# Kernel tuning notes

Hardware: AMD Instinct MI355X
Metric: run time of the kernel (lower is better)

The kernel has to match this reference:

```python
import jax, jax.numpy as jnp
import numpy as np

B, S, T, D = 4, 512, 512, 256


def setup_inputs() -> dict:
    key = jax.random.key(0)
    ks = jax.random.split(key, 10)
    scale = 1.0 / np.sqrt(D)
    return {
        "source": jax.random.normal(ks[0], (B, S, D), jnp.float32),
        "target": jax.random.normal(ks[1], (B, T, D), jnp.float32),
        "W_src": jax.random.uniform(ks[2], (D, D), jnp.float32, -scale, scale),
        "b_src": jax.random.uniform(ks[3], (D,), jnp.float32, -scale, scale),
        "W_tgt": jax.random.uniform(ks[4], (D, D), jnp.float32, -scale, scale),
        "b_tgt": jax.random.uniform(ks[5], (D,), jnp.float32, -scale, scale),
        "W_res": jax.random.uniform(ks[6], (D, 1), jnp.float32, -scale, scale),
        "b_res": jax.random.uniform(ks[7], (1,), jnp.float32, -scale, scale),
        "W_prob": jax.random.uniform(ks[8], (D, 2), jnp.float32, -scale, scale),
        "b_prob": jax.random.uniform(ks[9], (2,), jnp.float32, -scale, scale),
    }


def reference(source, target, W_src, b_src, W_tgt, b_tgt, W_res, b_res, W_prob, b_prob):
    # source: (B,S,D), target: (B,T,D)
    src_lin = jnp.einsum("bsd,de->bse", source, W_src) + b_src  # (B,S,D)
    tgt_lin = jnp.einsum("btd,de->bte", target, W_tgt) + b_tgt  # (B,T,D)
    # Bahdanau-style additive attention: (B,T,S,D) broadcast, tanh, D->1
    h = jnp.tanh(src_lin[:, None, :, :] + tgt_lin[:, :, None, :])  # (B,T,S,D)
    genP = jnp.einsum("btsd,d->bts", h, W_res[:, 0]) + b_res[0]     # (B,T,S)
    prob = jax.nn.softmax(jnp.einsum("btd,de->bte", target, W_prob) + b_prob, axis=-1)  # (B,T,2)
    return genP, prob
```

## Files before the change

### kernel.cpp

```cpp
#include <hip/hip_runtime.h>

#define B_ 4
#define S_ 512
#define T_ 512
#define D_ 256
#define NSRC (B_ * S_)
#define K2F 2.8853900817779268f

typedef __attribute__((ext_vector_type(8))) short short8;
typedef __attribute__((ext_vector_type(4))) float f32x4;

__device__ __forceinline__ unsigned short f2bf(float f) {
    union { float f; unsigned u; } v; v.f = f;
    unsigned r = v.u + 0x7FFF + ((v.u >> 16) & 1);
    return (unsigned short)(r >> 16);
}

__global__ __launch_bounds__(256) void prep_kernel(
    const float* __restrict__ src, const float* __restrict__ tgt,
    const float* __restrict__ Wsrc, const float* __restrict__ Wtgt,
    const float* __restrict__ Wp, const float* __restrict__ bp,
    unsigned short* __restrict__ abf, unsigned short* __restrict__ wtb,
    float* __restrict__ out)
{
    __shared__ float tl[64 * 65];
    const int blk = blockIdx.x, tid = threadIdx.x;

    if (blk < 1024) {
        int i4 = blk * 256 + tid;
        const int half = NSRC * D_ / 4;
        const float4* in = (i4 < half) ? (const float4*)src : (const float4*)tgt;
        int j = (i4 < half) ? i4 : i4 - half;
        float4 v = in[j];
        ushort4 o;
        o.x = f2bf(v.x); o.y = f2bf(v.y); o.z = f2bf(v.z); o.w = f2bf(v.w);
        *(ushort4*)&abf[i4 * 4] = o;
    } else if (blk < 1056) {
        int wb = blk - 1024;
        int e = wb >> 4, ti = wb & 15, tr = ti >> 2, tc = ti & 3;
        int r0 = tr * 64, c0 = tc * 64;
        const float* W = e ? Wtgt : Wsrc;
        #pragma unroll
        for (int it = 0; it < 4; it++) {
            int rr = (tid >> 4) + it * 16;
            int cc = (tid & 15) * 4;
            float4 v = *(const float4*)&W[(r0 + rr) * D_ + c0 + cc];
            tl[(cc + 0) * 65 + rr] = v.x;
            tl[(cc + 1) * 65 + rr] = v.y;
            tl[(cc + 2) * 65 + rr] = v.z;
            tl[(cc + 3) * 65 + rr] = v.w;
        }
        __syncthreads();
        #pragma unroll
        for (int it = 0; it < 2; it++) {
            int jj = (tid >> 3) + it * 32;
            int kk = (tid & 7) * 8;
            ushort4 lo, hi;
            lo.x = f2bf(tl[jj * 65 + kk + 0]); lo.y = f2bf(tl[jj * 65 + kk + 1]);
            lo.z = f2bf(tl[jj * 65 + kk + 2]); lo.w = f2bf(tl[jj * 65 + kk + 3]);
            hi.x = f2bf(tl[jj * 65 + kk + 4]); hi.y = f2bf(tl[jj * 65 + kk + 5]);
            hi.z = f2bf(tl[jj * 65 + kk + 6]); hi.w = f2bf(tl[jj * 65 + kk + 7]);
            int idx = (e * 256 + c0 + jj) * D_ + r0 + kk;
            *(ushort4*)&wtb[idx] = lo;
            *(ushort4*)&wtb[idx + 4] = hi;
        }
    } else {
        int row  = (blk - 1056) * 4 + (tid >> 6);
        int lane = tid & 63;
        float p0 = 0.f, p1 = 0.f;
        #pragma unroll
        for (int i = 0; i < 4; i++) {
            int d = lane + i * 64;
            float v = tgt[row * D_ + d];
            float2 w = *(const float2*)&Wp[d * 2];
            p0 = fmaf(v, w.x, p0);
            p1 = fmaf(v, w.y, p1);
        }
        #pragma unroll
        for (int off = 32; off > 0; off >>= 1) {
            p0 += __shfl_down(p0, off, 64);
            p1 += __shfl_down(p1, off, 64);
        }
        if (lane == 0) {
            const float L2E = 1.4426950408889634f;
            float l0 = p0 + bp[0], l1 = p1 + bp[1];
            float e10 = __builtin_amdgcn_exp2f((l1 - l0) * L2E);
            float e01 = __builtin_amdgcn_exp2f((l0 - l1) * L2E);
            out[B_ * T_ * S_ + row * 2 + 0] = __builtin_amdgcn_rcpf(1.f + e10);
            out[B_ * T_ * S_ + row * 2 + 1] = __builtin_amdgcn_rcpf(1.f + e01);
        }
    }
}

__global__ __launch_bounds__(256, 1) void mega_kernel(
    const unsigned short* __restrict__ abf, const unsigned short* __restrict__ wtb,
    const float* __restrict__ bsrc, const float* __restrict__ btgt,
    const float* __restrict__ Wres, const float* __restrict__ bres,
    float* __restrict__ out)
{
    __shared__ float ls[64 * 68];
    __shared__ float lt[64 * 68];
    __shared__ float wl[D_];
    __shared__ float c0s;

    const int tid = threadIdx.x;
    const int lane = tid & 63, w = tid >> 6;
    const int s0 = blockIdx.x * 64;
    const int t0 = blockIdx.y * 64;
    const int b  = blockIdx.z;

    wl[tid] = Wres[tid];
    if (w == 0) {
        float s = Wres[lane] + Wres[lane + 64] + Wres[lane + 128] + Wres[lane + 192];
        #pragma unroll
        for (int off = 32; off > 0; off >>= 1) s += __shfl_xor(s, off, 64);
        if (lane == 0) c0s = s + bres[0];
    }

    const int mat  = w >> 1;
    const int half = w & 1;
    const int n = lane & 15, quad = lane >> 4;
    const float* bias = mat ? btgt : bsrc;
    float* lx = mat ? lt : ls;
    const int R = mat ? (NSRC + b * T_ + t0) : (b * S_ + s0);

    short8 af[4][8];
    #pragma unroll
    for (int rg = 0; rg < 4; rg++)
        #pragma unroll
        for (int ks = 0; ks < 8; ks++)
            af[rg][ks] = *(const short8*)&abf[(R + rg * 16 + n) * D_ + ks * 32 + quad * 8];

    const int m = tid & 15;
    const int g = tid >> 4;
    float acc[4][4];
    #pragma unroll
    for (int i = 0; i < 4; i++)
        #pragma unroll
        for (int j = 0; j < 4; j++) acc[i][j] = 0.f;

    for (int c = 0; c < 4; c++) {
        #pragma unroll
        for (int cgi = 0; cgi < 2; cgi++) {
            const int cg = half * 2 + cgi;
            const int gcol = c * 4 + cg;
            const unsigned short* bptr = &wtb[(mat * 256 + gcol * 16 + n) * D_ + quad * 8];
            short8 bf[8];
            #pragma unroll
            for (int ks = 0; ks < 8; ks++) bf[ks] = *(const short8*)&bptr[ks * 32];
            const int dloc = cg * 16 + n;
            const float bv = bias[gcol * 16 + n];
            #pragma unroll
            for (int rg = 0; rg < 4; rg++) {
                f32x4 a4 = {0.f, 0.f, 0.f, 0.f};
                #pragma unroll
                for (int ks = 0; ks < 8; ks++)
                    a4 = __builtin_amdgcn_mfma_f32_16x16x32_bf16(af[rg][ks], bf[ks], a4, 0, 0, 0);
                float4 o;
                o.x = __builtin_amdgcn_exp2f((a4[0] + bv) * K2F);
                o.y = __builtin_amdgcn_exp2f((a4[1] + bv) * K2F);
                o.z = __builtin_amdgcn_exp2f((a4[2] + bv) * K2F);
                o.w = __builtin_amdgcn_exp2f((a4[3] + bv) * K2F);
                *(float4*)&lx[dloc * 68 + rg * 16 + quad * 4] = o;
            }
        }
        __syncthreads();

        const float* wp = &wl[c * 64];
        #pragma unroll 8
        for (int k = 0; k < 64; k++) {
            float4 av = *(const float4*)&ls[k * 68 + 4 * m];
            float4 cv = *(const float4*)&lt[k * 68 + 4 * g];
            float wv = wp[k];
            float a0 = av.x, a1 = av.y, a2 = av.z, a3 = av.w;
            float c0 = cv.x, c1 = cv.y, c2 = cv.z, c3 = cv.w;
            float r;
            r = __builtin_amdgcn_rcpf(fmaf(c0, a0, 1.f)); acc[0][0] = fmaf(wv, r, acc[0][0]);
            r = __builtin_amdgcn_rcpf(fmaf(c0, a1, 1.f)); acc[0][1] = fmaf(wv, r, acc[0][1]);
            r = __builtin_amdgcn_rcpf(fmaf(c0, a2, 1.f)); acc[0][2] = fmaf(wv, r, acc[0][2]);
            r = __builtin_amdgcn_rcpf(fmaf(c0, a3, 1.f)); acc[0][3] = fmaf(wv, r, acc[0][3]);
            r = __builtin_amdgcn_rcpf(fmaf(c1, a0, 1.f)); acc[1][0] = fmaf(wv, r, acc[1][0]);
            r = __builtin_amdgcn_rcpf(fmaf(c1, a1, 1.f)); acc[1][1] = fmaf(wv, r, acc[1][1]);
            r = __builtin_amdgcn_rcpf(fmaf(c1, a2, 1.f)); acc[1][2] = fmaf(wv, r, acc[1][2]);
            r = __builtin_amdgcn_rcpf(fmaf(c1, a3, 1.f)); acc[1][3] = fmaf(wv, r, acc[1][3]);
            r = __builtin_amdgcn_rcpf(fmaf(c2, a0, 1.f)); acc[2][0] = fmaf(wv, r, acc[2][0]);
            r = __builtin_amdgcn_rcpf(fmaf(c2, a1, 1.f)); acc[2][1] = fmaf(wv, r, acc[2][1]);
            r = __builtin_amdgcn_rcpf(fmaf(c2, a2, 1.f)); acc[2][2] = fmaf(wv, r, acc[2][2]);
            r = __builtin_amdgcn_rcpf(fmaf(c2, a3, 1.f)); acc[2][3] = fmaf(wv, r, acc[2][3]);
            r = __builtin_amdgcn_rcpf(fmaf(c3, a0, 1.f)); acc[3][0] = fmaf(wv, r, acc[3][0]);
            r = __builtin_amdgcn_rcpf(fmaf(c3, a1, 1.f)); acc[3][1] = fmaf(wv, r, acc[3][1]);
            r = __builtin_amdgcn_rcpf(fmaf(c3, a2, 1.f)); acc[3][2] = fmaf(wv, r, acc[3][2]);
            r = __builtin_amdgcn_rcpf(fmaf(c3, a3, 1.f)); acc[3][3] = fmaf(wv, r, acc[3][3]);
        }
        __syncthreads();
    }

    const float C0 = c0s;
    #pragma unroll
    for (int i = 0; i < 4; i++) {
        float4 o;
        o.x = C0 - 2.f * acc[i][0];
        o.y = C0 - 2.f * acc[i][1];
        o.z = C0 - 2.f * acc[i][2];
        o.w = C0 - 2.f * acc[i][3];
        *(float4*)&out[(b * T_ + t0 + 4 * g + i) * S_ + s0 + 4 * m] = o;
    }
}

extern "C" void kernel_launch(void* const* d_in, const int* in_sizes, int n_in,
                              void* d_out, int out_size, void* d_ws, size_t ws_size,
                              hipStream_t stream) {
    const float* source = (const float*)d_in[0];
    const float* target = (const float*)d_in[1];
    const float* W_src  = (const float*)d_in[2];
    const float* b_src  = (const float*)d_in[3];
    const float* W_tgt  = (const float*)d_in[4];
    const float* b_tgt  = (const float*)d_in[5];
    const float* W_res  = (const float*)d_in[6];
    const float* b_res  = (const float*)d_in[7];
    const float* W_prob = (const float*)d_in[8];
    const float* b_prob = (const float*)d_in[9];
    float* out = (float*)d_out;

    unsigned short* abf = (unsigned short*)d_ws;
    unsigned short* wtb = abf + 2 * NSRC * D_;

    prep_kernel<<<1568, 256, 0, stream>>>(source, target, W_src, W_tgt,
                                          W_prob, b_prob, abf, wtb, out);
    mega_kernel<<<dim3(8, 8, 4), 256, 0, stream>>>(abf, wtb, b_src, b_tgt,
                                                   W_res, b_res, out);
}
```

Before: 126.5 us.

## Halve target tile to 32 rows, rebalance MFMA work across waves, double occupancy

Shrinks each block's target tile from 64 to 32 rows, doubling the grid to 512 blocks so all CUs get work. The source/target projection work is repartitioned: two waves handle 64 source rows (two row groups each) and two waves handle 32 target rows, each covering all columns of a chunk. Launch bounds allow two blocks per CU, Wres is read from global instead of LDS, and each thread now accumulates a 2x4 output tile. The trade-off is that the source projection is recomputed twice as often across blocks.

Measured after the change: 139.4 us. +10.2%, slower.

```diff
diff --git a/kernel.cpp b/kernel.cpp
--- a/kernel.cpp
+++ b/kernel.cpp
@@ -92,24 +92,54 @@
     }
 }
 
-__global__ __launch_bounds__(256, 1) void mega_kernel(
+template<int NRG, int LDSTR>
+__device__ __forceinline__ void do_phaseA(
+    const short8 (&af)[2][8], const unsigned short* __restrict__ wtbase,
+    const float* __restrict__ bias, float* lx, int c, int n, int quad)
+{
+    #pragma unroll
+    for (int cg = 0; cg < 4; cg++) {
+        const int gcol = c * 4 + cg;
+        const unsigned short* bptr = &wtbase[(gcol * 16 + n) * D_ + quad * 8];
+        short8 bf[8];
+        #pragma unroll
+        for (int ks = 0; ks < 8; ks++) bf[ks] = *(const short8*)&bptr[ks * 32];
+        const int dloc = cg * 16 + n;
+        const float bv = bias[gcol * 16 + n];
+        #pragma unroll
+        for (int j = 0; j < NRG; j++) {
+            f32x4 a4 = {0.f, 0.f, 0.f, 0.f};
+            #pragma unroll
+            for (int ks = 0; ks < 8; ks++)
+                a4 = __builtin_amdgcn_mfma_f32_16x16x32_bf16(af[j][ks], bf[ks], a4, 0, 0, 0);
+            float4 o;
+            o.x = __builtin_amdgcn_exp2f((a4[0] + bv) * K2F);
+            o.y = __builtin_amdgcn_exp2f((a4[1] + bv) * K2F);
+            o.z = __builtin_amdgcn_exp2f((a4[2] + bv) * K2F);
+            o.w = __builtin_amdgcn_exp2f((a4[3] + bv) * K2F);
+            *(float4*)&lx[dloc * LDSTR + j * 16 + quad * 4] = o;
+        }
+    }
+}
+
+#define LSTR 68
+#define TSTR 36
+__global__ __launch_bounds__(256, 2) void mega_kernel(
     const unsigned short* __restrict__ abf, const unsigned short* __restrict__ wtb,
     const float* __restrict__ bsrc, const float* __restrict__ btgt,
     const float* __restrict__ Wres, const float* __restrict__ bres,
     float* __restrict__ out)
 {
-    __shared__ float ls[64 * 68];
-    __shared__ float lt[64 * 68];
-    __shared__ float wl[D_];
+    __shared__ float ls[64 * LSTR];
+    __shared__ float lt[64 * TSTR];
     __shared__ float c0s;
 
     const int tid = threadIdx.x;
     const int lane = tid & 63, w = tid >> 6;
     const int s0 = blockIdx.x * 64;
-    const int t0 = blockIdx.y * 64;
+    const int t0 = blockIdx.y * 32;
     const int b  = blockIdx.z;
 
-    wl[tid] = Wres[tid];
     if (w == 0) {
         float s = Wres[lane] + Wres[lane + 64] + Wres[lane + 128] + Wres[lane + 192];
         #pragma unroll
@@ -117,63 +147,45 @@
         if (lane == 0) c0s = s + bres[0];
     }
 
-    const int mat  = w >> 1;
-    const int half = w & 1;
+    const int mat = w >> 1;
+    const int h   = w & 1;
     const int n = lane & 15, quad = lane >> 4;
-    const float* bias = mat ? btgt : bsrc;
-    float* lx = mat ? lt : ls;
-    const int R = mat ? (NSRC + b * T_ + t0) : (b * S_ + s0);
-
-    short8 af[4][8];
-    #pragma unroll
-    for (int rg = 0; rg < 4; rg++)
+    const int rgbase = mat ? h : 2 * h;
+    const int R0 = mat ? (NSRC + b * T_ + t0) : (b * S_ + s0);
+
+    short8 af[2][8];
+    #pragma unroll
+    for (int ks = 0; ks < 8; ks++)
+        af[0][ks] = *(const short8*)&abf[(R0 + rgbase * 16 + n) * D_ + ks * 32 + quad * 8];
+    if (mat == 0) {
         #pragma unroll
         for (int ks = 0; ks < 8; ks++)
-            af[rg][ks] = *(const short8*)&abf[(R + rg * 16 + n) * D_ + ks * 32 + quad * 8];
+            af[1][ks] = *(const short8*)&abf[(R0 + (rgbase + 1) * 16 + n) * D_ + ks * 32 + quad * 8];
+    }
 
     const int m = tid & 15;
     const int g = tid >> 4;
-    float acc[4][4];
-    #pragma unroll
-    for (int i = 0; i < 4; i++)
+    float acc[2][4];
+    #pragma unroll
+    for (int i = 0; i < 2; i++)
         #pragma unroll
         for (int j = 0; j < 4; j++) acc[i][j] = 0.f;
 
     for (int c = 0; c < 4; c++) {
-        #pragma unroll
-        for (int cgi = 0; cgi < 2; cgi++) {
-            const int cg = half * 2 + cgi;
-            const int gcol = c * 4 + cg;
-            const unsigned short* bptr = &wtb[(mat * 256 + gcol * 16 + n) * D_ + quad * 8];
-            short8 bf[8];
-            #pragma unroll
-            for (int ks = 0; ks < 8; ks++) bf[ks] = *(const short8*)&bptr[ks * 32];
-            const int dloc = cg * 16 + n;
-            const float bv = bias[gcol * 16 + n];
-            #pragma unroll
-            for (int rg = 0; rg < 4; rg++) {
-                f32x4 a4 = {0.f, 0.f, 0.f, 0.f};
-                #pragma unroll
-                for (int ks = 0; ks < 8; ks++)
-                    a4 = __builtin_amdgcn_mfma_f32_16x16x32_bf16(af[rg][ks], bf[ks], a4, 0, 0, 0);
-                float4 o;
-                o.x = __builtin_amdgcn_exp2f((a4[0] + bv) * K2F);
-                o.y = __builtin_amdgcn_exp2f((a4[1] + bv) * K2F);
-                o.z = __builtin_amdgcn_exp2f((a4[2] + bv) * K2F);
-                o.w = __builtin_amdgcn_exp2f((a4[3] + bv) * K2F);
-                *(float4*)&lx[dloc * 68 + rg * 16 + quad * 4] = o;
-            }
-        }
+        if (mat == 0)
+            do_phaseA<2, LSTR>(af, wtb, bsrc, ls + rgbase * 16, c, n, quad);
+        else
+            do_phaseA<1, TSTR>(af, wtb + 256 * D_, btgt, lt + rgbase * 16, c, n, quad);
         __syncthreads();
 
-        const float* wp = &wl[c * 64];
+        const float* wp = &Wres[c * 64];
         #pragma unroll 8
         for (int k = 0; k < 64; k++) {
-            float4 av = *(const float4*)&ls[k * 68 + 4 * m];
-            float4 cv = *(const float4*)&lt[k * 68 + 4 * g];
+            float4 av = *(const float4*)&ls[k * LSTR + 4 * m];
+            float2 cv = *(const float2*)&lt[k * TSTR + 2 * g];
             float wv = wp[k];
             float a0 = av.x, a1 = av.y, a2 = av.z, a3 = av.w;
-            float c0 = cv.x, c1 = cv.y, c2 = cv.z, c3 = cv.w;
+            float c0 = cv.x, c1 = cv.y;
             float r;
             r = __builtin_amdgcn_rcpf(fmaf(c0, a0, 1.f)); acc[0][0] = fmaf(wv, r, acc[0][0]);
             r = __builtin_amdgcn_rcpf(fmaf(c0, a1, 1.f)); acc[0][1] = fmaf(wv, r, acc[0][1]);
@@ -183,27 +195,19 @@
             r = __builtin_amdgcn_rcpf(fmaf(c1, a1, 1.f)); acc[1][1] = fmaf(wv, r, acc[1][1]);
             r = __builtin_amdgcn_rcpf(fmaf(c1, a2, 1.f)); acc[1][2] = fmaf(wv, r, acc[1][2]);
             r = __builtin_amdgcn_rcpf(fmaf(c1, a3, 1.f)); acc[1][3] = fmaf(wv, r, acc[1][3]);
-            r = __builtin_amdgcn_rcpf(fmaf(c2, a0, 1.f)); acc[2][0] = fmaf(wv, r, acc[2][0]);
-            r = __builtin_amdgcn_rcpf(fmaf(c2, a1, 1.f)); acc[2][1] = fmaf(wv, r, acc[2][1]);
-            r = __builtin_amdgcn_rcpf(fmaf(c2, a2, 1.f)); acc[2][2] = fmaf(wv, r, acc[2][2]);
-            r = __builtin_amdgcn_rcpf(fmaf(c2, a3, 1.f)); acc[2][3] = fmaf(wv, r, acc[2][3]);
-            r = __builtin_amdgcn_rcpf(fmaf(c3, a0, 1.f)); acc[3][0] = fmaf(wv, r, acc[3][0]);
-            r = __builtin_amdgcn_rcpf(fmaf(c3, a1, 1.f)); acc[3][1] = fmaf(wv, r, acc[3][1]);
-            r = __builtin_amdgcn_rcpf(fmaf(c3, a2, 1.f)); acc[3][2] = fmaf(wv, r, acc[3][2]);
-            r = __builtin_amdgcn_rcpf(fmaf(c3, a3, 1.f)); acc[3][3] = fmaf(wv, r, acc[3][3]);
         }
         __syncthreads();
     }
 
     const float C0 = c0s;
     #pragma unroll
-    for (int i = 0; i < 4; i++) {
+    for (int i = 0; i < 2; i++) {
         float4 o;
         o.x = C0 - 2.f * acc[i][0];
         o.y = C0 - 2.f * acc[i][1];
         o.z = C0 - 2.f * acc[i][2];
         o.w = C0 - 2.f * acc[i][3];
-        *(float4*)&out[(b * T_ + t0 + 4 * g + i) * S_ + s0 + 4 * m] = o;
+        *(float4*)&out[(b * T_ + t0 + 2 * g + i) * S_ + s0 + 4 * m] = o;
     }
 }
 
@@ -227,6 +231,6 @@
 
     prep_kernel<<<1568, 256, 0, stream>>>(source, target, W_src, W_tgt,
                                           W_prob, b_prob, abf, wtb, out);
-    mega_kernel<<<dim3(8, 8, 4), 256, 0, stream>>>(abf, wtb, b_src, b_tgt,
-                                                   W_res, b_res, out);
-}
+    mega_kernel<<<dim3(8, 16, 4), 256, 0, stream>>>(abf, wtb, b_src, b_tgt,
+                                                    W_res, b_res, out);
+}
```

## Double-buffer LDS tiles to overlap MFMA projection with tanh-reduction loop

Applied to the files above, without the earlier changes.

Splits the shared-memory tiles into two buffers so the MFMA projection and exp step for the next 64-column chunk is issued before the reciprocal-accumulate loop over the current chunk. This is meant to hide the projection latency behind the rcp/fma work. It also changes the wave split: each wave now covers two row groups across all four column groups instead of four row groups across two, and it reads W_res straight from global memory instead of staging it in LDS. The cost is twice the LDS footprint and a different register-pressure profile. The per-iteration barrier placement is not fully visible, so buffer synchronisation correctness is uncertain.

After: 125.6 us. About the same (-0.7%).

```diff
diff --git a/kernel.cpp b/kernel.cpp
--- a/kernel.cpp
+++ b/kernel.cpp
@@ -92,15 +92,15 @@
     }
 }
 
+#define LSTR 68
 __global__ __launch_bounds__(256, 1) void mega_kernel(
     const unsigned short* __restrict__ abf, const unsigned short* __restrict__ wtb,
     const float* __restrict__ bsrc, const float* __restrict__ btgt,
     const float* __restrict__ Wres, const float* __restrict__ bres,
     float* __restrict__ out)
 {
-    __shared__ float ls[64 * 68];
-    __shared__ float lt[64 * 68];
-    __shared__ float wl[D_];
+    __shared__ float ls[2][64 * LSTR];
+    __shared__ float lt[2][64 * LSTR];
     __shared__ float c0s;
 
     const int tid = threadIdx.x;
@@ -109,7 +109,6 @@
     const int t0 = blockIdx.y * 64;
     const int b  = blockIdx.z;
 
-    wl[tid] = Wres[tid];
     if (w == 0) {
         float s = Wres[lane] + Wres[lane + 64] + Wres[lane + 128] + Wres[lane + 192];
         #pragma unroll
@@ -117,19 +116,19 @@
         if (lane == 0) c0s = s + bres[0];
     }
 
-    const int mat  = w >> 1;
-    const int half = w & 1;
+    const int mat = w >> 1;
+    const int rb  = 2 * (w & 1);
     const int n = lane & 15, quad = lane >> 4;
     const float* bias = mat ? btgt : bsrc;
-    float* lx = mat ? lt : ls;
-    const int R = mat ? (NSRC + b * T_ + t0) : (b * S_ + s0);
-
-    short8 af[4][8];
+    const unsigned short* wtbase = wtb + mat * 256 * D_;
+    const int R0 = mat ? (NSRC + b * T_ + t0) : (b * S_ + s0);
+
+    short8 af[2][8];
     #pragma unroll
-    for (int rg = 0; rg < 4; rg++)
+    for (int rg = 0; rg < 2; rg++)
         #pragma unroll
         for (int ks = 0; ks < 8; ks++)
-            af[rg][ks] = *(const short8*)&abf[(R + rg * 16 + n) * D_ + ks * 32 + quad * 8];
+            af[rg][ks] = *(const short8*)&abf[(R0 + (rb + rg) * 16 + n) * D_ + ks * 32 + quad * 8];
 
     const int m = tid & 15;
     const int g = tid >> 4;
@@ -139,19 +138,19 @@
         #pragma unroll
         for (int j = 0; j < 4; j++) acc[i][j] = 0.f;
 
-    for (int c = 0; c < 4; c++) {
-        #pragma unroll
-        for (int cgi = 0; cgi < 2; cgi++) {
-            const int cg = half * 2 + cgi;
+    auto phaseA = [&](int c, int bi) {
+        float* lx = (mat ? lt[bi] : ls[bi]);
+        #pragma unroll
+        for (int cg = 0; cg < 4; cg++) {
             const int gcol = c * 4 + cg;
-            const unsigned short* bptr = &wtb[(mat * 256 + gcol * 16 + n) * D_ + quad * 8];
+            const unsigned short* bptr = &wtbase[(gcol * 16 + n) * D_ + quad * 8];
             short8 bf[8];
             #pragma unroll
             for (int ks = 0; ks < 8; ks++) bf[ks] = *(const short8*)&bptr[ks * 32];
             const int dloc = cg * 16 + n;
             const float bv = bias[gcol * 16 + n];
             #pragma unroll
-            for (int rg = 0; rg < 4; rg++) {
+            for (int rg = 0; rg < 2; rg++) {
                 f32x4 a4 = {0.f, 0.f, 0.f, 0.f};
                 #pragma unroll
                 for (int ks = 0; ks < 8; ks++)
@@ -161,16 +160,25 @@
                 o.y = __builtin_amdgcn_exp2f((a4[1] + bv) * K2F);
                 o.z = __builtin_amdgcn_exp2f((a4[2] + bv) * K2F);
                 o.w = __builtin_amdgcn_exp2f((a4[3] + bv) * K2F);
-                *(float4*)&lx[dloc * 68 + rg * 16 + quad * 4] = o;
+                *(float4*)&lx[dloc * LSTR + (rb + rg) * 16 + quad * 4] = o;
             }
         }
-        __syncthreads();
-
-        const float* wp = &wl[c * 64];
+    };
+
+    phaseA(0, 0);
+    __syncthreads();
+
+    for (int c = 0; c < 4; c++) {
+        const int bi = c & 1;
+        if (c < 3) phaseA(c + 1, bi ^ 1);
+
+        const float* lsb = ls[bi];
+        const float* ltb = lt[bi];
+        const float* wp = &Wres[c * 64];
         #pragma unroll 8
         for (int k = 0; k < 64; k++) {
-            float4 av = *(const float4*)&ls[k * 68 + 4 * m];
-            float4 cv = *(const float4*)&lt[k * 68 + 4 * g];
+            float4 av = *(const float4*)&lsb[k * LSTR + 4 * m];
+            float4 cv = *(const float4*)&ltb[k * LSTR + 4 * g];
             float wv = wp[k];
             float a0 = av.x, a1 = av.y, a2 = av.z, a3 = av.w;
             float c0 = cv.x, c1 = cv.y, c2 = cv.z, c3 = cv.w;
```
